# Kernel tuning notes

Hardware: AMD Instinct MI355X
Metric: run time of the kernel (lower is better)

The kernel has to match this reference:

```python
import jax, jax.numpy as jnp
import numpy as np

B, K, C = 1024, 8, 10   # predicted points, concepts, classes per concept
N = 8192                # background (training) set size
EPS = 1e-13


def setup_inputs() -> dict:
    key = jax.random.key(0)
    k1, k2, k3 = jax.random.split(key, 3)
    c_p = jax.random.normal(k1, (B, K, C), dtype=jnp.float32)
    bandwidth = jnp.ones((K * C,), dtype=jnp.float32)  # learned param, init 1.0
    c_in = jax.random.randint(k2, (N, K), 0, C, dtype=jnp.int64)
    delta_in = jax.random.randint(k3, (N,), 0, 2, dtype=jnp.int32)
    return {"c_p": c_p, "bandwidth": bandwidth, "c_in": c_in, "delta_in": delta_in}


def _beran(c_p, bandwidth, c_in, delta_in):
    # ---- GaussKernel l2 metric ----
    proba = jax.nn.softmax(c_p, axis=-1)                      # [B,K,C]
    bw = jnp.clip(bandwidth, 0.001, 10.0).reshape(K, C)       # [K,C]
    onehot = jax.nn.one_hot(c_in, C, dtype=proba.dtype)       # [N,K,C]
    # sum((p - l)^2 / bw) = sum(p^2/bw) - 2 sum(p*l/bw) + sum(l^2/bw)
    A = jnp.sum(proba * proba / bw, axis=(1, 2))              # [B]
    D = jnp.einsum('nkc,kc->n', onehot, 1.0 / bw)             # [N]
    cross = jnp.einsum('bkc,nkc->bn', proba / bw, onehot)     # [B,N]
    metric = A[:, None] - 2.0 * cross + D[None, :]            # [B,N]
    weights = jnp.exp(-metric)
    s = jnp.sum(weights, axis=1, keepdims=True)               # normalize over background axis
    bad = s < EPS
    W = jnp.where(bad, 0.0, weights / jnp.where(bad, 1.0, s)) # [B,N]

    # ---- Beran cumulative hazard scan ----
    w_cumsum = jnp.cumsum(W, axis=1)
    shifted = w_cumsum - W
    ones = jnp.ones_like(shifted)
    bad2 = jnp.isclose(shifted, ones) | jnp.isclose(w_cumsum, ones)
    shifted = jnp.where(bad2, 0.0, shifted)
    w_cumsum = jnp.where(bad2, 0.0, w_cumsum)
    xi = jnp.log(1.0 - shifted) - jnp.log(1.0 - w_cumsum)
    filtered_xi = delta_in.astype(xi.dtype)[None, :] * xi
    hazards = jnp.cumsum(filtered_xi, axis=1)
    surv_func = jnp.exp(-hazards)                             # [B,N]
    first_step = 1.0 - surv_func[:, :1]
    surv_steps = jnp.concatenate([first_step, surv_func[:, :-1] - surv_func[:, 1:]], axis=1)
    ss = jnp.sum(surv_steps, axis=1, keepdims=True)
    bad3 = ss < EPS
    surv_steps = jnp.where(bad3, 0.0, surv_steps / jnp.where(bad3, 1.0, ss))
    return surv_func, surv_steps


def reference(c_p, bandwidth, c_in, delta_in):
    return _beran(c_p, bandwidth, c_in, delta_in)
```

## Files before the change

### kernel.cpp

```cpp
#include <hip/hip_runtime.h>

#define NN 8192
#define BB 1024
#define KK 8
#define CC 10
#define NT 512
#define CHUNK (NN/NT)
#define NW (NT/64)

__device__ __forceinline__ int swz(int n) {
    return (n & ~31) | ((n + (n >> 5)) & 31);
}

__global__ void pack_kernel(const int* __restrict__ c_in, const int* __restrict__ delta_in,
                            unsigned* __restrict__ pairs, unsigned* __restrict__ dmask_g) {
    int n = blockIdx.x * blockDim.x + threadIdx.x;
    if (n >= NN) return;
    const int4* p = reinterpret_cast<const int4*>(c_in + (size_t)n * KK);
    int4 lo = p[0], hi = p[1];
    unsigned p0 = (unsigned)(lo.x * 10 + lo.y);
    unsigned p1 = (unsigned)(lo.z * 10 + lo.w);
    unsigned p2 = (unsigned)(hi.x * 10 + hi.y);
    unsigned p3 = (unsigned)(hi.z * 10 + hi.w);
    pairs[n] = p0 | (p1 << 7) | (p2 << 14) | (p3 << 21);
    unsigned long long bal = __ballot(delta_in[n] & 1);
    if ((threadIdx.x & 63) == 0) {
        dmask_g[n >> 5]       = (unsigned)(bal & 0xffffffffull);
        dmask_g[(n >> 5) + 1] = (unsigned)(bal >> 32);
    }
}

__device__ __forceinline__ float block_excl_scan(float v, int lane, int wv, float* ws,
                                                 float* total) {
    float x = v;
    #pragma unroll
    for (int d = 1; d < 64; d <<= 1) {
        float y = __shfl_up(x, d);
        if (lane >= d) x += y;
    }
    if (lane == 63) ws[wv] = x;
    __syncthreads();
    float off = x - v, tot = 0.0f;
    #pragma unroll
    for (int w = 0; w < NW; w++) {
        float y = ws[w];
        tot += y;
        if (w < wv) off += y;
    }
    *total = tot;
    return off;
}

__global__ __launch_bounds__(NT, 8) void beran_kernel(
    const float* __restrict__ c_p, const float* __restrict__ bandwidth,
    const int* __restrict__ c_in, const int* __restrict__ delta_in,
    const unsigned* __restrict__ pairs, const unsigned* __restrict__ dmask_g,
    float* __restrict__ out)
{
    __shared__ float a[NN];
    __shared__ float ttab[KK * CC];
    __shared__ float ttab2[4 * 100];
    __shared__ float Apart[KK];
    __shared__ float wsB[NW];
    __shared__ float wsC[NW];

    const int b    = blockIdx.x;
    const int t    = threadIdx.x;
    const int lane = t & 63;
    const int wv   = t >> 6;
    const int base = t * CHUNK;

    if (t < KK) {
        const int k = t;
        float v[CC];
        float mx = -1e30f;
        #pragma unroll
        for (int c = 0; c < CC; c++) { v[c] = c_p[((size_t)b*KK + k)*CC + c]; mx = fmaxf(mx, v[c]); }
        float se = 0.0f;
        #pragma unroll
        for (int c = 0; c < CC; c++) { v[c] = __expf(v[c] - mx); se += v[c]; }
        float inv = 1.0f / se;
        float Ak = 0.0f;
        #pragma unroll
        for (int c = 0; c < CC; c++) {
            float p  = v[c] * inv;
            float bw = bandwidth[k*CC + c];
            bw = fminf(fmaxf(bw, 0.001f), 10.0f);
            float ib = 1.0f / bw;
            ttab[k*CC + c] = ib - 2.0f * p * ib;
            Ak += p * p * ib;
        }
        Apart[k] = Ak;
    }
    __syncthreads();
    if (t < 400) {
        int k = t / 100, p = t % 100;
        ttab2[t] = ttab[(k*2)*CC + p/10] + ttab[(k*2+1)*CC + p%10];
    }
    float A = 0.0f;
    #pragma unroll
    for (int k = 0; k < KK; k++) A += Apart[k];
    __syncthreads();

    float creg[CHUNK];
    unsigned dm = 0;
    float run = 0.0f;
    if (pairs) {
        {
            unsigned dm32 = dmask_g[t >> 1];
            dm = (dm32 >> ((t & 1) * 16)) & 0xffffu;
        }
        #pragma unroll
        for (int g = 0; g < CHUNK / 4; g++) {
            uint4 pk = *reinterpret_cast<const uint4*>(pairs + base + g * 4);
#define DOPAIR(pw, idx) { \
            float m = A + ttab2[(pw) & 127] + ttab2[100 + (((pw) >> 7) & 127)] \
                    + ttab2[200 + (((pw) >> 14) & 127)] + ttab2[300 + ((pw) >> 21)]; \
            run += __expf(-m); creg[idx] = run; }
            DOPAIR(pk.x, g*4 + 0)
            DOPAIR(pk.y, g*4 + 1)
            DOPAIR(pk.z, g*4 + 2)
            DOPAIR(pk.w, g*4 + 3)
#undef DOPAIR
        }
    } else {
        #pragma unroll
        for (int i = 0; i < CHUNK; i++) {
            const int4* p4 = reinterpret_cast<const int4*>(c_in + (size_t)(base + i) * KK);
            int4 lo4 = p4[0], hi4 = p4[1];
            float m = A;
            m += ttab[0*CC + lo4.x] + ttab[1*CC + lo4.y] + ttab[2*CC + lo4.z] + ttab[3*CC + lo4.w];
            m += ttab[4*CC + hi4.x] + ttab[5*CC + hi4.y] + ttab[6*CC + hi4.z] + ttab[7*CC + hi4.w];
            run += __expf(-m);
            creg[i] = run;
            dm |= (unsigned)(delta_in[base + i] & 1) << i;
        }
    }

    float s;
    const float off_raw = block_excl_scan(run, lane, wv, wsB, &s);
    const float invs = (s < 1e-13f) ? 0.0f : 1.0f / s;

    const float ISO = 1.00001e-5f;
    float csprev = off_raw * invs;
    float Lprev  = __logf(1.0f - csprev);
    float run2 = 0.0f;
    #pragma unroll
    for (int i = 0; i < CHUNK; i++) {
        float cs = (creg[i] + off_raw) * invs;
        float L  = __logf(1.0f - cs);
        bool bad = (fabsf(csprev - 1.0f) <= ISO) || (fabsf(cs - 1.0f) <= ISO);
        float xi = bad ? 0.0f : (Lprev - L);
        float f  = ((dm >> i) & 1u) ? xi : 0.0f;
        run2 += f;
        creg[i] = run2;
        csprev = cs;
        Lprev  = L;
    }

    float H;
    const float off2 = block_excl_scan(run2, lane, wv, wsC, &H);

    #pragma unroll
    for (int i = 0; i < CHUNK; i++) a[swz(base + i)] = __expf(-(creg[i] + off2));
    __syncthreads();

    const float surv_last = a[swz(NN - 1)];
    const float ss = 1.0f - surv_last;
    const float invss = (ss < 1e-13f) ? 0.0f : 1.0f / ss;
    float* outS = out + (size_t)b * NN;
    float* outT = out + (size_t)BB * NN + (size_t)b * NN;
    #pragma unroll
    for (int j = 0; j < NN / (NT * 4); j++) {
        int n0 = j * NT * 4 + t * 4;
        float s0 = a[swz(n0)];
        float s1 = a[swz(n0 + 1)];
        float s2 = a[swz(n0 + 2)];
        float s3 = a[swz(n0 + 3)];
        float sp = (n0 == 0) ? 1.0f : a[swz(n0 - 1)];
        *reinterpret_cast<float4*>(outS + n0) = make_float4(s0, s1, s2, s3);
        *reinterpret_cast<float4*>(outT + n0) =
            make_float4((sp - s0) * invss, (s0 - s1) * invss,
                        (s1 - s2) * invss, (s2 - s3) * invss);
    }
}

extern "C" void kernel_launch(void* const* d_in, const int* in_sizes, int n_in,
                              void* d_out, int out_size, void* d_ws, size_t ws_size,
                              hipStream_t stream) {
    const float* c_p       = (const float*)d_in[0];
    const float* bandwidth = (const float*)d_in[1];
    const int*   c_in      = (const int*)d_in[2];
    const int*   delta_in  = (const int*)d_in[3];
    float* out = (float*)d_out;

    unsigned* pairs   = nullptr;
    unsigned* dmask_g = nullptr;
    const size_t need = (size_t)NN * sizeof(unsigned) + (size_t)(NN / 32) * sizeof(unsigned);
    if (ws_size >= need) {
        pairs   = (unsigned*)d_ws;
        dmask_g = (unsigned*)((char*)d_ws + (size_t)NN * sizeof(unsigned));
        pack_kernel<<<NN / 256, 256, 0, stream>>>(c_in, delta_in, pairs, dmask_g);
    }
    beran_kernel<<<BB, NT, 0, stream>>>(c_p, bandwidth, c_in, delta_in, pairs, dmask_g, out);
}
```

Before: 28.95 us.

## Process two rows per block with three-way grouped lookup tables

After: 31.66 us. +9.3%, slower.

```diff
diff --git a/kernel.cpp b/kernel.cpp
--- a/kernel.cpp
+++ b/kernel.cpp
@@ -5,8 +5,11 @@
 #define KK 8
 #define CC 10
 #define NT 512
+#define ROWS 2
+#define GRID (BB/ROWS)
 #define CHUNK (NN/NT)
 #define NW (NT/64)
+#define T3SZ 2100
 
 __device__ __forceinline__ int swz(int n) {
     return (n & ~31) | ((n + (n >> 5)) & 31);
@@ -18,11 +21,10 @@
     if (n >= NN) return;
     const int4* p = reinterpret_cast<const int4*>(c_in + (size_t)n * KK);
     int4 lo = p[0], hi = p[1];
-    unsigned p0 = (unsigned)(lo.x * 10 + lo.y);
-    unsigned p1 = (unsigned)(lo.z * 10 + lo.w);
-    unsigned p2 = (unsigned)(hi.x * 10 + hi.y);
-    unsigned p3 = (unsigned)(hi.z * 10 + hi.w);
-    pairs[n] = p0 | (p1 << 7) | (p2 << 14) | (p3 << 21);
+    unsigned g0 = (unsigned)((lo.x * 10 + lo.y) * 10 + lo.z);
+    unsigned g1 = (unsigned)((lo.w * 10 + hi.x) * 10 + hi.y);
+    unsigned g2 = (unsigned)(hi.z * 10 + hi.w);
+    pairs[n] = g0 | (g1 << 10) | (g2 << 20);
     unsigned long long bal = __ballot(delta_in[n] & 1);
     if ((threadIdx.x & 63) == 0) {
         dmask_g[n >> 5]       = (unsigned)(bal & 0xffffffffull);
@@ -51,27 +53,27 @@
     return off;
 }
 
-__global__ __launch_bounds__(NT, 8) void beran_kernel(
+__global__ __launch_bounds__(NT, 4) void beran_kernel(
     const float* __restrict__ c_p, const float* __restrict__ bandwidth,
     const int* __restrict__ c_in, const int* __restrict__ delta_in,
     const unsigned* __restrict__ pairs, const unsigned* __restrict__ dmask_g,
     float* __restrict__ out)
 {
     __shared__ float a[NN];
-    __shared__ float ttab[KK * CC];
-    __shared__ float ttab2[4 * 100];
-    __shared__ float Apart[KK];
-    __shared__ float wsB[NW];
-    __shared__ float wsC[NW];
-
-    const int b    = blockIdx.x;
+    __shared__ float tb[ROWS][KK * CC];
+    __shared__ float Apart[ROWS][KK];
+    __shared__ float t3[ROWS][T3SZ];
+    __shared__ float wss[ROWS][2][NW];
+
     const int t    = threadIdx.x;
     const int lane = t & 63;
     const int wv   = t >> 6;
     const int base = t * CHUNK;
-
-    if (t < KK) {
-        const int k = t;
+    const int b0   = blockIdx.x * ROWS;
+
+    if (t < ROWS * KK) {
+        const int r = t >> 3, k = t & 7;
+        const int b = b0 + r;
         float v[CC];
         float mx = -1e30f;
         #pragma unroll
@@ -87,101 +89,118 @@
             float bw = bandwidth[k*CC + c];
             bw = fminf(fmaxf(bw, 0.001f), 10.0f);
             float ib = 1.0f / bw;
-            ttab[k*CC + c] = ib - 2.0f * p * ib;
+            tb[r][k*CC + c] = ib - 2.0f * p * ib;
             Ak += p * p * ib;
         }
-        Apart[k] = Ak;
+        Apart[r][k] = Ak;
     }
     __syncthreads();
-    if (t < 400) {
-        int k = t / 100, p = t % 100;
-        ttab2[t] = ttab[(k*2)*CC + p/10] + ttab[(k*2+1)*CC + p%10];
-    }
-    float A = 0.0f;
-    #pragma unroll
-    for (int k = 0; k < KK; k++) A += Apart[k];
+
+    for (int e = t; e < ROWS * T3SZ; e += NT) {
+        const int r = e / T3SZ;
+        const int i = e - r * T3SZ;
+        float v;
+        if (i < 1000) {
+            v = tb[r][0*CC + i/100] + tb[r][1*CC + (i/10)%10] + tb[r][2*CC + i%10];
+        } else if (i < 2000) {
+            int j = i - 1000;
+            v = tb[r][3*CC + j/100] + tb[r][4*CC + (j/10)%10] + tb[r][5*CC + j%10];
+        } else {
+            int q = i - 2000;
+            float Ar = 0.0f;
+            #pragma unroll
+            for (int k = 0; k < KK; k++) Ar += Apart[r][k];
+            v = tb[r][6*CC + q/10] + tb[r][7*CC + q%10] + Ar;
+        }
+        t3[r][i] = -v;
+    }
     __syncthreads();
 
-    float creg[CHUNK];
+    unsigned pk[CHUNK];
     unsigned dm = 0;
-    float run = 0.0f;
     if (pairs) {
-        {
-            unsigned dm32 = dmask_g[t >> 1];
-            dm = (dm32 >> ((t & 1) * 16)) & 0xffffu;
-        }
         #pragma unroll
         for (int g = 0; g < CHUNK / 4; g++) {
-            uint4 pk = *reinterpret_cast<const uint4*>(pairs + base + g * 4);
-#define DOPAIR(pw, idx) { \
-            float m = A + ttab2[(pw) & 127] + ttab2[100 + (((pw) >> 7) & 127)] \
-                    + ttab2[200 + (((pw) >> 14) & 127)] + ttab2[300 + ((pw) >> 21)]; \
-            run += __expf(-m); creg[idx] = run; }
-            DOPAIR(pk.x, g*4 + 0)
-            DOPAIR(pk.y, g*4 + 1)
-            DOPAIR(pk.z, g*4 + 2)
-            DOPAIR(pk.w, g*4 + 3)
-#undef DOPAIR
-        }
+            uint4 v = *reinterpret_cast<const uint4*>(pairs + base + g * 4);
+            pk[g*4+0] = v.x; pk[g*4+1] = v.y; pk[g*4+2] = v.z; pk[g*4+3] = v.w;
+        }
+        unsigned dm32 = dmask_g[t >> 1];
+        dm = (dm32 >> ((t & 1) * 16)) & 0xffffu;
     } else {
         #pragma unroll
         for (int i = 0; i < CHUNK; i++) {
             const int4* p4 = reinterpret_cast<const int4*>(c_in + (size_t)(base + i) * KK);
-            int4 lo4 = p4[0], hi4 = p4[1];
-            float m = A;
-            m += ttab[0*CC + lo4.x] + ttab[1*CC + lo4.y] + ttab[2*CC + lo4.z] + ttab[3*CC + lo4.w];
-            m += ttab[4*CC + hi4.x] + ttab[5*CC + hi4.y] + ttab[6*CC + hi4.z] + ttab[7*CC + hi4.w];
-            run += __expf(-m);
+            int4 lo = p4[0], hi = p4[1];
+            unsigned g0 = (unsigned)((lo.x * 10 + lo.y) * 10 + lo.z);
+            unsigned g1 = (unsigned)((lo.w * 10 + hi.x) * 10 + hi.y);
+            unsigned g2 = (unsigned)(hi.z * 10 + hi.w);
+            pk[i] = g0 | (g1 << 10) | (g2 << 20);
+            dm |= (unsigned)(delta_in[base + i] & 1) << i;
+        }
+    }
+
+    #pragma unroll
+    for (int r = 0; r < ROWS; r++) {
+        const float* t3r = t3[r];
+
+        float creg[CHUNK];
+        float run = 0.0f;
+        #pragma unroll
+        for (int i = 0; i < CHUNK; i++) {
+            unsigned w0 = pk[i];
+            float m = t3r[w0 & 1023] + t3r[1000 + ((w0 >> 10) & 1023)]
+                    + t3r[2000 + (w0 >> 20)];
+            run += __expf(m);
             creg[i] = run;
-            dm |= (unsigned)(delta_in[base + i] & 1) << i;
-        }
-    }
-
-    float s;
-    const float off_raw = block_excl_scan(run, lane, wv, wsB, &s);
-    const float invs = (s < 1e-13f) ? 0.0f : 1.0f / s;
-
-    const float ISO = 1.00001e-5f;
-    float csprev = off_raw * invs;
-    float Lprev  = __logf(1.0f - csprev);
-    float run2 = 0.0f;
-    #pragma unroll
-    for (int i = 0; i < CHUNK; i++) {
-        float cs = (creg[i] + off_raw) * invs;
-        float L  = __logf(1.0f - cs);
-        bool bad = (fabsf(csprev - 1.0f) <= ISO) || (fabsf(cs - 1.0f) <= ISO);
-        float xi = bad ? 0.0f : (Lprev - L);
-        float f  = ((dm >> i) & 1u) ? xi : 0.0f;
-        run2 += f;
-        creg[i] = run2;
-        csprev = cs;
-        Lprev  = L;
-    }
-
-    float H;
-    const float off2 = block_excl_scan(run2, lane, wv, wsC, &H);
-
-    #pragma unroll
-    for (int i = 0; i < CHUNK; i++) a[swz(base + i)] = __expf(-(creg[i] + off2));
-    __syncthreads();
-
-    const float surv_last = a[swz(NN - 1)];
-    const float ss = 1.0f - surv_last;
-    const float invss = (ss < 1e-13f) ? 0.0f : 1.0f / ss;
-    float* outS = out + (size_t)b * NN;
-    float* outT = out + (size_t)BB * NN + (size_t)b * NN;
-    #pragma unroll
-    for (int j = 0; j < NN / (NT * 4); j++) {
-        int n0 = j * NT * 4 + t * 4;
-        float s0 = a[swz(n0)];
-        float s1 = a[swz(n0 + 1)];
-        float s2 = a[swz(n0 + 2)];
-        float s3 = a[swz(n0 + 3)];
-        float sp = (n0 == 0) ? 1.0f : a[swz(n0 - 1)];
-        *reinterpret_cast<float4*>(outS + n0) = make_float4(s0, s1, s2, s3);
-        *reinterpret_cast<float4*>(outT + n0) =
-            make_float4((sp - s0) * invss, (s0 - s1) * invss,
-                        (s1 - s2) * invss, (s2 - s3) * invss);
+        }
+
+        float s;
+        const float off_raw = block_excl_scan(run, lane, wv, wss[r][0], &s);
+        const float invs = (s < 1e-13f) ? 0.0f : 1.0f / s;
+
+        const float ISO = 1.00001e-5f;
+        float csprev = off_raw * invs;
+        float Lprev  = __logf(1.0f - csprev);
+        float run2 = 0.0f;
+        #pragma unroll
+        for (int i = 0; i < CHUNK; i++) {
+            float cs = (creg[i] + off_raw) * invs;
+            float L  = __logf(1.0f - cs);
+            bool bad = (fabsf(csprev - 1.0f) <= ISO) || (fabsf(cs - 1.0f) <= ISO);
+            float xi = bad ? 0.0f : (Lprev - L);
+            float f  = ((dm >> i) & 1u) ? xi : 0.0f;
+            run2 += f;
+            creg[i] = run2;
+            csprev = cs;
+            Lprev  = L;
+        }
+
+        float H;
+        const float off2 = block_excl_scan(run2, lane, wv, wss[r][1], &H);
+
+        #pragma unroll
+        for (int i = 0; i < CHUNK; i++) a[swz(base + i)] = __expf(-(creg[i] + off2));
+        __syncthreads();
+
+        const float surv_last = a[swz(NN - 1)];
+        const float ss = 1.0f - surv_last;
+        const float invss = (ss < 1e-13f) ? 0.0f : 1.0f / ss;
+        const int b = b0 + r;
+        float* outS = out + (size_t)b * NN;
+        float* outT = out + (size_t)BB * NN + (size_t)b * NN;
+        #pragma unroll
+        for (int j = 0; j < NN / (NT * 4); j++) {
+            int n0 = j * NT * 4 + t * 4;
+            float s0 = a[swz(n0)];
+            float s1 = a[swz(n0 + 1)];
+            float s2 = a[swz(n0 + 2)];
+            float s3 = a[swz(n0 + 3)];
+            float sp = (n0 == 0) ? 1.0f : a[swz(n0 - 1)];
+            *reinterpret_cast<float4*>(outS + n0) = make_float4(s0, s1, s2, s3);
+            *reinterpret_cast<float4*>(outT + n0) =
+                make_float4((sp - s0) * invss, (s0 - s1) * invss,
+                            (s1 - s2) * invss, (s2 - s3) * invss);
+        }
     }
 }
 
@@ -202,5 +221,5 @@
         dmask_g = (unsigned*)((char*)d_ws + (size_t)NN * sizeof(unsigned));
         pack_kernel<<<NN / 256, 256, 0, stream>>>(c_in, delta_in, pairs, dmask_g);
     }
-    beran_kernel<<<BB, NT, 0, stream>>>(c_p, bandwidth, c_in, delta_in, pairs, dmask_g, out);
-}
+    beran_kernel<<<GRID, NT, 0, stream>>>(c_p, bandwidth, c_in, delta_in, pairs, dmask_g, out);
+}
```

## Use triple-lookup tables, multiplicative survival scan, and shuffle-based output staging

Applied to the files above, without the earlier changes.

Measured after the change: 32.71 us. 1.13x slower.

```diff
diff --git a/kernel.cpp b/kernel.cpp
--- a/kernel.cpp
+++ b/kernel.cpp
@@ -4,13 +4,10 @@
 #define BB 1024
 #define KK 8
 #define CC 10
-#define NT 512
+#define NT 1024
 #define CHUNK (NN/NT)
 #define NW (NT/64)
-
-__device__ __forceinline__ int swz(int n) {
-    return (n & ~31) | ((n + (n >> 5)) & 31);
-}
+#define T3SZ 2100
 
 __global__ void pack_kernel(const int* __restrict__ c_in, const int* __restrict__ delta_in,
                             unsigned* __restrict__ pairs, unsigned* __restrict__ dmask_g) {
@@ -18,37 +15,15 @@
     if (n >= NN) return;
     const int4* p = reinterpret_cast<const int4*>(c_in + (size_t)n * KK);
     int4 lo = p[0], hi = p[1];
-    unsigned p0 = (unsigned)(lo.x * 10 + lo.y);
-    unsigned p1 = (unsigned)(lo.z * 10 + lo.w);
-    unsigned p2 = (unsigned)(hi.x * 10 + hi.y);
-    unsigned p3 = (unsigned)(hi.z * 10 + hi.w);
-    pairs[n] = p0 | (p1 << 7) | (p2 << 14) | (p3 << 21);
+    unsigned g0 = (unsigned)((lo.x * 10 + lo.y) * 10 + lo.z);
+    unsigned g1 = (unsigned)((lo.w * 10 + hi.x) * 10 + hi.y);
+    unsigned g2 = (unsigned)(hi.z * 10 + hi.w);
+    pairs[n] = g0 | (g1 << 10) | (g2 << 20);
     unsigned long long bal = __ballot(delta_in[n] & 1);
     if ((threadIdx.x & 63) == 0) {
         dmask_g[n >> 5]       = (unsigned)(bal & 0xffffffffull);
         dmask_g[(n >> 5) + 1] = (unsigned)(bal >> 32);
     }
-}
-
-__device__ __forceinline__ float block_excl_scan(float v, int lane, int wv, float* ws,
-                                                 float* total) {
-    float x = v;
-    #pragma unroll
-    for (int d = 1; d < 64; d <<= 1) {
-        float y = __shfl_up(x, d);
-        if (lane >= d) x += y;
-    }
-    if (lane == 63) ws[wv] = x;
-    __syncthreads();
-    float off = x - v, tot = 0.0f;
-    #pragma unroll
-    for (int w = 0; w < NW; w++) {
-        float y = ws[w];
-        tot += y;
-        if (w < wv) off += y;
-    }
-    *total = tot;
-    return off;
 }
 
 __global__ __launch_bounds__(NT, 8) void beran_kernel(
@@ -57,12 +32,11 @@
     const unsigned* __restrict__ pairs, const unsigned* __restrict__ dmask_g,
     float* __restrict__ out)
 {
-    __shared__ float a[NN];
-    __shared__ float ttab[KK * CC];
-    __shared__ float ttab2[4 * 100];
+    __shared__ float tb[KK * CC];
     __shared__ float Apart[KK];
-    __shared__ float wsB[NW];
-    __shared__ float wsC[NW];
+    __shared__ float t3[T3SZ];
+    __shared__ float wsA[NW];
+    __shared__ float wsM[NW];
 
     const int b    = blockIdx.x;
     const int t    = threadIdx.x;
@@ -87,97 +61,142 @@
             float bw = bandwidth[k*CC + c];
             bw = fminf(fmaxf(bw, 0.001f), 10.0f);
             float ib = 1.0f / bw;
-            ttab[k*CC + c] = ib - 2.0f * p * ib;
+            tb[k*CC + c] = ib - 2.0f * p * ib;
             Ak += p * p * ib;
         }
         Apart[k] = Ak;
     }
     __syncthreads();
-    if (t < 400) {
-        int k = t / 100, p = t % 100;
-        ttab2[t] = ttab[(k*2)*CC + p/10] + ttab[(k*2+1)*CC + p%10];
-    }
-    float A = 0.0f;
-    #pragma unroll
-    for (int k = 0; k < KK; k++) A += Apart[k];
+
+    for (int i = t; i < T3SZ; i += NT) {
+        float v;
+        if (i < 1000) {
+            v = tb[0*CC + i/100] + tb[1*CC + (i/10)%10] + tb[2*CC + i%10];
+        } else if (i < 2000) {
+            int j = i - 1000;
+            v = tb[3*CC + j/100] + tb[4*CC + (j/10)%10] + tb[5*CC + j%10];
+        } else {
+            int q = i - 2000;
+            float Ar = 0.0f;
+            #pragma unroll
+            for (int k = 0; k < KK; k++) Ar += Apart[k];
+            v = tb[6*CC + q/10] + tb[7*CC + q%10] + Ar;
+        }
+        t3[i] = -v;
+    }
     __syncthreads();
 
     float creg[CHUNK];
     unsigned dm = 0;
     float run = 0.0f;
     if (pairs) {
-        {
-            unsigned dm32 = dmask_g[t >> 1];
-            dm = (dm32 >> ((t & 1) * 16)) & 0xffffu;
-        }
-        #pragma unroll
-        for (int g = 0; g < CHUNK / 4; g++) {
-            uint4 pk = *reinterpret_cast<const uint4*>(pairs + base + g * 4);
-#define DOPAIR(pw, idx) { \
-            float m = A + ttab2[(pw) & 127] + ttab2[100 + (((pw) >> 7) & 127)] \
-                    + ttab2[200 + (((pw) >> 14) & 127)] + ttab2[300 + ((pw) >> 21)]; \
-            run += __expf(-m); creg[idx] = run; }
-            DOPAIR(pk.x, g*4 + 0)
-            DOPAIR(pk.y, g*4 + 1)
-            DOPAIR(pk.z, g*4 + 2)
-            DOPAIR(pk.w, g*4 + 3)
-#undef DOPAIR
+        dm = (dmask_g[t >> 2] >> ((t & 3) * 8)) & 0xffu;
+        uint4 v0 = *reinterpret_cast<const uint4*>(pairs + base);
+        uint4 v1 = *reinterpret_cast<const uint4*>(pairs + base + 4);
+        unsigned pk[CHUNK] = {v0.x, v0.y, v0.z, v0.w, v1.x, v1.y, v1.z, v1.w};
+        #pragma unroll
+        for (int i = 0; i < CHUNK; i++) {
+            unsigned w0 = pk[i];
+            float m = t3[w0 & 1023] + t3[1000 + ((w0 >> 10) & 1023)]
+                    + t3[2000 + (w0 >> 20)];
+            run += __expf(m);
+            creg[i] = run;
         }
     } else {
+        float A = 0.0f;
+        #pragma unroll
+        for (int k = 0; k < KK; k++) A += Apart[k];
         #pragma unroll
         for (int i = 0; i < CHUNK; i++) {
             const int4* p4 = reinterpret_cast<const int4*>(c_in + (size_t)(base + i) * KK);
-            int4 lo4 = p4[0], hi4 = p4[1];
+            int4 lo = p4[0], hi = p4[1];
             float m = A;
-            m += ttab[0*CC + lo4.x] + ttab[1*CC + lo4.y] + ttab[2*CC + lo4.z] + ttab[3*CC + lo4.w];
-            m += ttab[4*CC + hi4.x] + ttab[5*CC + hi4.y] + ttab[6*CC + hi4.z] + ttab[7*CC + hi4.w];
+            m += tb[0*CC + lo.x] + tb[1*CC + lo.y] + tb[2*CC + lo.z] + tb[3*CC + lo.w];
+            m += tb[4*CC + hi.x] + tb[5*CC + hi.y] + tb[6*CC + hi.z] + tb[7*CC + hi.w];
             run += __expf(-m);
             creg[i] = run;
             dm |= (unsigned)(delta_in[base + i] & 1) << i;
         }
     }
 
-    float s;
-    const float off_raw = block_excl_scan(run, lane, wv, wsB, &s);
+    float x = run;
+    #pragma unroll
+    for (int d = 1; d < 64; d <<= 1) {
+        float y = __shfl_up(x, d);
+        if (lane >= d) x += y;
+    }
+    if (lane == 63) wsA[wv] = x;
+    __syncthreads();
+    float excl = __shfl_up(x, 1);
+    if (lane == 0) excl = 0.0f;
+    float s = 0.0f, woff = 0.0f;
+    #pragma unroll
+    for (int w = 0; w < NW; w++) {
+        float y = wsA[w];
+        s += y;
+        if (w < wv) woff += y;
+    }
+    const float off_raw = woff + excl;
     const float invs = (s < 1e-13f) ? 0.0f : 1.0f / s;
 
     const float ISO = 1.00001e-5f;
-    float csprev = off_raw * invs;
-    float Lprev  = __logf(1.0f - csprev);
-    float run2 = 0.0f;
+    float uprev = 1.0f - off_raw * invs;
+    float P = 1.0f;
     #pragma unroll
     for (int i = 0; i < CHUNK; i++) {
         float cs = (creg[i] + off_raw) * invs;
-        float L  = __logf(1.0f - cs);
-        bool bad = (fabsf(csprev - 1.0f) <= ISO) || (fabsf(cs - 1.0f) <= ISO);
-        float xi = bad ? 0.0f : (Lprev - L);
-        float f  = ((dm >> i) & 1u) ? xi : 0.0f;
-        run2 += f;
-        creg[i] = run2;
-        csprev = cs;
-        Lprev  = L;
-    }
-
-    float H;
-    const float off2 = block_excl_scan(run2, lane, wv, wsC, &H);
-
-    #pragma unroll
-    for (int i = 0; i < CHUNK; i++) a[swz(base + i)] = __expf(-(creg[i] + off2));
-    __syncthreads();
-
-    const float surv_last = a[swz(NN - 1)];
+        float u  = 1.0f - cs;
+        bool bad  = (fabsf(uprev) <= ISO) || (fabsf(u) <= ISO);
+        bool flag = (dm >> i) & 1u;
+        float f = (flag && !bad) ? u * __builtin_amdgcn_rcpf(uprev) : 1.0f;
+        P *= f;
+        creg[i] = P;
+        uprev = u;
+    }
+
+    float xm = P;
+    #pragma unroll
+    for (int d = 1; d < 64; d <<= 1) {
+        float y = __shfl_up(xm, d);
+        if (lane >= d) xm *= y;
+    }
+    if (lane == 63) wsM[wv] = xm;
+    __syncthreads();
+    float exclm = __shfl_up(xm, 1);
+    if (lane == 0) exclm = 1.0f;
+    float tot = 1.0f, moff = 1.0f;
+    #pragma unroll
+    for (int w = 0; w < NW; w++) {
+        float y = wsM[w];
+        tot *= y;
+        if (w < wv) moff *= y;
+    }
+    const float S_base = moff * exclm;
+    const float surv_last = tot;
     const float ss = 1.0f - surv_last;
     const float invss = (ss < 1e-13f) ? 0.0f : 1.0f / ss;
+
+    #pragma unroll
+    for (int i = 0; i < CHUNK; i++) creg[i] = S_base * creg[i];
+
+    const float wave_base = __shfl(S_base, 0);
+    const float g1sp     = __shfl(creg[7], 31);
+
     float* outS = out + (size_t)b * NN;
     float* outT = out + (size_t)BB * NN + (size_t)b * NN;
-    #pragma unroll
-    for (int j = 0; j < NN / (NT * 4); j++) {
-        int n0 = j * NT * 4 + t * 4;
-        float s0 = a[swz(n0)];
-        float s1 = a[swz(n0 + 1)];
-        float s2 = a[swz(n0 + 2)];
-        float s3 = a[swz(n0 + 3)];
-        float sp = (n0 == 0) ? 1.0f : a[swz(n0 - 1)];
+    const bool hi = (lane & 1);
+    #pragma unroll
+    for (int g = 0; g < 2; g++) {
+        const int o = 32 * g + (lane >> 1);
+        float e0 = __shfl(creg[0], o), e1 = __shfl(creg[1], o);
+        float e2 = __shfl(creg[2], o), e3 = __shfl(creg[3], o);
+        float o0 = __shfl(creg[4], o), o1 = __shfl(creg[5], o);
+        float o2 = __shfl(creg[6], o), o3 = __shfl(creg[7], o);
+        float s0 = hi ? o0 : e0, s1 = hi ? o1 : e1;
+        float s2 = hi ? o2 : e2, s3 = hi ? o3 : e3;
+        float sp = __shfl_up(s3, 1);
+        if (lane == 0) sp = (g == 0) ? wave_base : g1sp;
+        const int n0 = wv * 512 + g * 256 + lane * 4;
         *reinterpret_cast<float4*>(outS + n0) = make_float4(s0, s1, s2, s3);
         *reinterpret_cast<float4*>(outT + n0) =
             make_float4((sp - s0) * invss, (s0 - s1) * invss,
```
